# Optimization experiments

Hardware: AMD Instinct MI355X
Metric: run time of the kernel (lower is better)

The kernel has to match this reference:

```python
import math
import jax, jax.numpy as jnp
import numpy as np

N, C, H, W = 32, 128, 56, 56


def unfold3(x, axis, dil):
    """F.unfold with 3-tap kernel along `axis`, dilation `dil`, padding `dil`.
    Input (n,c,h,w) -> output (n,c,3,h,w); tap k takes offset (k-1)*dil."""
    pad_cfg = [(0, 0)] * 4
    pad_cfg[axis] = (dil, dil)
    xp = jnp.pad(x, pad_cfg)
    size = x.shape[axis]
    taps = [jax.lax.slice_in_dim(xp, k * dil, k * dil + size, axis=axis) for k in range(3)]
    return jnp.stack(taps, axis=2)


def setup_inputs() -> dict:
    key = jax.random.key(0)
    k0, k1, k2, k3, k4 = jax.random.split(key, 5)
    x = jax.random.normal(k0, (N, C, H, W), dtype=jnp.float32)
    # trunc_normal_(std=0.02) approximated by normal * 0.02
    p2 = jax.random.normal(k1, (1, 1, 3, 1, W), dtype=jnp.float32) * 0.02
    # 1x1 conv weight (out=C, in=3C), kaiming-ish scale
    p3 = jax.random.normal(k2, (C, 3 * C), dtype=jnp.float32) * (1.0 / math.sqrt(3 * C))
    p5 = jax.random.normal(k3, (1, 1, H, W), dtype=jnp.float32) * 0.02
    p10 = jax.random.normal(k4, (1, C, 3, H, W), dtype=jnp.float32) * 0.02
    return {"x": x, "p2": p2, "p3": p3, "p5": p5, "p10": p10}


def reference(x, p2, p3, p5, p10):
    n, c, h, w = x.shape
    # t_1: vertical 3-tap unfold, dilation 2 -> (n,c,3,h,w)
    t1 = unfold3(x, axis=2, dil=2)
    t2 = p2 * t1                                              # (n,c,3,h,w)
    # t_3: 1x1 conv over the c*3 channel view
    t3 = jnp.einsum('nkhw,ck->nchw', t1.reshape(n, c * 3, h, w), p3)
    # t_4: horizontal 3-tap unfold, dilation 1
    t4 = unfold3(t3, axis=3, dil=1)                           # (n,c,3,h,w)
    t5 = p5 * t3                                              # (n,c,h,w)
    # t_7/t_8: horizontal 3-tap unfold of x, dilation 2, softmax over taps
    t7 = unfold3(x, axis=3, dil=2)
    t8 = jax.nn.softmax(t7, axis=2)                           # (n,c,3,h,w)
    # t_9: bmm over spatial dim -> (n,c,c*3)
    t9 = jnp.einsum('ncx,ndx->ncd', x.reshape(n, c, h * w),
                    t4.reshape(n, c * 3, h * w)) / math.sqrt(h * w)
    t10 = p10 * t8                                            # (n,c,3,h,w)
    # t_11: memory-reinterpreting view: (n,1,c,h,w) - (n,3,c,h,w) -> back to (n,c,3,h,w)
    t11 = (t5[:, None] - t2.reshape(n, 3, c, h, w)).reshape(n, c, 3, h, w)
    t12 = t11 - t10                                           # (n,c,3,h,w)
    # t_13: bmm over c*3 -> (n,c,h*w)
    t13 = jnp.einsum('ncd,ndx->ncx', t9,
                     t12.reshape(n, c * 3, h * w)) / math.sqrt(c * 3)
    return t13.reshape(n, c, h, w)
```

## Files before the change

### kernel.cpp

```cpp
#include <hip/hip_runtime.h>
#include <stdint.h>

#define NB 32
#define C_ 128
#define H_ 56
#define W_ 56
#define HW 3136
#define KD 384

typedef __attribute__((ext_vector_type(8))) short bf16x8;
typedef __attribute__((ext_vector_type(4))) float f32x4;

__device__ inline uint16_t f2bf(float f) {
    uint32_t u = __float_as_uint(f);
    return (uint16_t)((u + 0x7FFFu + ((u >> 16) & 1u)) >> 16);
}
__device__ inline float bf2f(uint16_t b) {
    return __uint_as_float(((uint32_t)b) << 16);
}

__global__ __launch_bounds__(256) void p1_xtp(const float* __restrict__ x,
                                              uint16_t* __restrict__ xtp,
                                              uint16_t* __restrict__ xb) {
    __shared__ uint16_t lt[56][136];
    const int h = blockIdx.x, n = blockIdx.y, tid = threadIdx.x;
    const int c = tid >> 1, wh = tid & 1;
    const float* xr = &x[(((size_t)n * C_ + c) * H_ + h) * W_ + wh * 28];
    uint32_t pk[14];
#pragma unroll
    for (int q = 0; q < 7; ++q) {
        float4 v = *(const float4*)&xr[q * 4];
        int wb = wh * 28 + q * 4;
        uint16_t b0 = f2bf(v.x), b1 = f2bf(v.y), b2 = f2bf(v.z), b3 = f2bf(v.w);
        lt[wb + 0][c] = b0;
        lt[wb + 1][c] = b1;
        lt[wb + 2][c] = b2;
        lt[wb + 3][c] = b3;
        pk[q * 2]     = (uint32_t)b0 | ((uint32_t)b1 << 16);
        pk[q * 2 + 1] = (uint32_t)b2 | ((uint32_t)b3 << 16);
    }
    {
        uint16_t* xrow = &xb[(((size_t)n * C_ + c) * H_ + h) * 64 + wh * 28];
#pragma unroll
        for (int q = 0; q < 7; ++q)
            *(uint2*)&xrow[q * 4] = make_uint2(pk[q * 2], pk[q * 2 + 1]);
        if (wh == 1) {
            uint4 z = {0, 0, 0, 0};
            *(uint4*)&xrow[28] = z;
        }
    }
    __syncthreads();
    const int w = tid >> 2, qc = tid & 3;
    uint16_t* dst = &xtp[((((size_t)n * H_ + h) * 64 + w)) * C_ + qc * 32];
    if (w < 56) {
        const uint32_t* s = (const uint32_t*)&lt[w][qc * 32];
        uint4 a = *(const uint4*)(s);
        uint4 b = *(const uint4*)(s + 4);
        uint4 c4 = *(const uint4*)(s + 8);
        uint4 d4 = *(const uint4*)(s + 12);
        *(uint4*)dst = a;
        *(uint4*)(dst + 8) = b;
        *(uint4*)(dst + 16) = c4;
        *(uint4*)(dst + 24) = d4;
    } else {
        uint4 z = {0, 0, 0, 0};
        *(uint4*)dst = z;
        *(uint4*)(dst + 8) = z;
        *(uint4*)(dst + 16) = z;
        *(uint4*)(dst + 24) = z;
    }
}

__global__ __launch_bounds__(256) void kpt(const float* __restrict__ p10,
                                           const float* __restrict__ p3,
                                           uint16_t* __restrict__ p10t,
                                           uint16_t* __restrict__ ap) {
    const int h = blockIdx.x, tid = threadIdx.x;
    for (int idx = tid; idx < 3072; idx += 256) {
        int w = idx & 63, ch = idx >> 6;
        int dp0 = ch * 8;
        uint32_t pk[4];
#pragma unroll
        for (int j = 0; j < 8; ++j) {
            int dp = dp0 + j;
            int tap = dp >> 7, c2 = dp & 127;
            int dor = 3 * c2 + tap;
            float v = (w < W_) ? p10[(size_t)dor * HW + h * W_ + w] : 0.f;
            uint16_t bb = f2bf(v);
            if (j & 1) pk[j >> 1] |= ((uint32_t)bb) << 16;
            else       pk[j >> 1] = bb;
        }
        *(uint4*)&p10t[((size_t)h * 64 + w) * KD + dp0] = *(const uint4*)pk;
    }
    for (int i = h * 256 + tid; i < 49152; i += 56 * 256) {
        int c = i / KD, dp = i - c * KD;
        int tap = dp >> 7, c2 = dp & 127;
        ap[i] = f2bf(p3[c * KD + 3 * c2 + tap]);
    }
}

__global__ __launch_bounds__(256) void k1(const uint16_t* __restrict__ xtp,
                                          const uint16_t* __restrict__ ap,
                                          uint16_t* __restrict__ t3b) {
    __shared__ uint16_t smem[3 * 32 * 128];
    const int bx = blockIdx.x, n = blockIdx.y, tid = threadIdx.x;
    const int h = bx >> 1, wbase = (bx & 1) << 5;
    const int lane = tid & 63, wid = tid >> 6;
    const int c15 = lane & 15, kq = lane >> 4;

    for (int t = tid; t < 1536; t += 256) {
        int tap = t >> 9, r = t & 511, w = r >> 4, qp = r & 15;
        int q = qp ^ (w & 7);
        int hh = h + 2 * (tap - 1);
        uint4 v = {0, 0, 0, 0};
        if ((unsigned)hh < (unsigned)H_)
            v = *(const uint4*)&xtp[((((size_t)n * H_ + hh) * 64 + wbase + w)) * C_ + q * 8];
        *(uint4*)&smem[tap * 4096 + w * 128 + qp * 8] = v;
    }
    __syncthreads();

    f32x4 acc[2][2] = {};
    for (int ks = 0; ks < 12; ++ks) {
        int tap = ks >> 2, kk = ks & 3;
        bf16x8 a[2], b[2];
#pragma unroll
        for (int m = 0; m < 2; ++m) {
            int c = wid * 32 + m * 16 + c15;
            a[m] = *(const bf16x8*)&ap[c * KD + ks * 32 + kq * 8];
        }
#pragma unroll
        for (int nt = 0; nt < 2; ++nt) {
            int w = nt * 16 + c15;
            int q = kk * 4 + kq;
            b[nt] = *(const bf16x8*)&smem[tap * 4096 + w * 128 + (q ^ (w & 7)) * 8];
        }
#pragma unroll
        for (int m = 0; m < 2; ++m)
#pragma unroll
            for (int nt = 0; nt < 2; ++nt)
                acc[m][nt] = __builtin_amdgcn_mfma_f32_16x16x32_bf16(a[m], b[nt], acc[m][nt], 0, 0, 0);
    }
    __syncthreads();

    uint16_t* lrow = smem;
#pragma unroll
    for (int m = 0; m < 2; ++m)
#pragma unroll
        for (int nt = 0; nt < 2; ++nt)
#pragma unroll
            for (int r = 0; r < 4; ++r) {
                int c = wid * 32 + m * 16 + kq * 4 + r;
                int wl = nt * 16 + c15;
                lrow[c * 40 + wl] = f2bf(acc[m][nt][r]);
            }
    __syncthreads();

    const uint32_t* lrowd = (const uint32_t*)smem;
    for (int t = tid; t < 512; t += 256) {
        int c = t >> 2, ch = t & 3;
        int m0 = c * 20 + ch * 4;
        uint4 o = make_uint4(lrowd[m0], lrowd[m0 + 1], lrowd[m0 + 2], lrowd[m0 + 3]);
        *(uint4*)&t3b[(((size_t)n * C_ + c) * H_ + h) * 64 + wbase + ch * 8] = o;
    }
}

__global__ __launch_bounds__(512) void k2(const uint16_t* __restrict__ xb,
                                          const uint16_t* __restrict__ t3b,
                                          uint16_t* __restrict__ part16) {
    __shared__ uint16_t xs[32 * 64];
    __shared__ uint16_t ts[128 * 64];
    const int bx = blockIdx.x;
    const int hc = bx >> 2, cq = bx & 3;
    const int n = blockIdx.y;
    const int tid = threadIdx.x, lane = tid & 63, wid = tid >> 6;
    const int c15 = lane & 15, kq = lane >> 4;

    f32x4 acc[2][3] = {};
    for (int hr = 0; hr < 8; ++hr) {
        const int h = hc * 8 + hr;
        __syncthreads();
        if (tid < 256) {
            int cl = tid >> 3, qp = tid & 7, q = qp ^ (cl & 7);
            uint4 v = *(const uint4*)&xb[(((size_t)n * C_ + cq * 32 + cl) * H_ + h) * 64 + q * 8];
            *(uint4*)&xs[cl * 64 + qp * 8] = v;
        }
        for (int t = tid; t < 1024; t += 512) {
            int c2 = t >> 3, qp = t & 7, q = qp ^ (c2 & 7);
            uint4 v = *(const uint4*)&t3b[(((size_t)n * C_ + c2) * H_ + h) * 64 + q * 8];
            *(uint4*)&ts[c2 * 64 + qp * 8] = v;
        }
        __syncthreads();
#pragma unroll
        for (int ks = 0; ks < 2; ++ks) {
            const int q = ks * 4 + kq;
            bf16x8 a[2];
#pragma unroll
            for (int m = 0; m < 2; ++m) {
                int cl = m * 16 + c15;
                a[m] = *(const bf16x8*)&xs[cl * 64 + ((q ^ (cl & 7)) << 3)];
            }
            const int c2 = wid * 16 + c15;
            const int base = c2 * 64;
            const int s7 = c2 & 7;
            uint4 v = *(const uint4*)&ts[base + ((q ^ s7) << 3)];
            uint32_t pv = (q > 0) ? *(const uint32_t*)&ts[base + (((q - 1) ^ s7) << 3) + 6] : 0u;
            uint32_t nx = (q < 7) ? *(const uint32_t*)&ts[base + (((q + 1) ^ s7) << 3)] : 0u;
            uint4 b0, b2;
            b0.x = (v.x << 16) | (pv >> 16);
            b0.y = (v.y << 16) | (v.x >> 16);
            b0.z = (v.z << 16) | (v.y >> 16);
            b0.w = (v.w << 16) | (v.z >> 16);
            b2.x = (v.y << 16) | (v.x >> 16);
            b2.y = (v.z << 16) | (v.y >> 16);
            b2.z = (v.w << 16) | (v.z >> 16);
            b2.w = (nx << 16)  | (v.w >> 16);
            bf16x8 bt0 = *(const bf16x8*)&b0;
            bf16x8 bt1 = *(const bf16x8*)&v;
            bf16x8 bt2 = *(const bf16x8*)&b2;
#pragma unroll
            for (int m = 0; m < 2; ++m) {
                acc[m][0] = __builtin_amdgcn_mfma_f32_16x16x32_bf16(a[m], bt0, acc[m][0], 0, 0, 0);
                acc[m][1] = __builtin_amdgcn_mfma_f32_16x16x32_bf16(a[m], bt1, acc[m][1], 0, 0, 0);
                acc[m][2] = __builtin_amdgcn_mfma_f32_16x16x32_bf16(a[m], bt2, acc[m][2], 0, 0, 0);
            }
        }
    }
#pragma unroll
    for (int m = 0; m < 2; ++m)
#pragma unroll
        for (int tap = 0; tap < 3; ++tap)
#pragma unroll
            for (int r = 0; r < 4; ++r) {
                int c = cq * 32 + m * 16 + kq * 4 + r;
                int dp = tap * 128 + wid * 16 + c15;
                part16[((size_t)(hc * NB + n) * C_ + c) * 384 + dp] = f2bf(acc[m][tap][r]);
            }
}

__global__ __launch_bounds__(256) void kra(const uint16_t* __restrict__ part16,
                                           uint16_t* __restrict__ acat) {
    __shared__ uint16_t lds[4][384];
    const int tid = threadIdx.x;
    const int rl = tid >> 6, lane = tid & 63;
    const int nc = blockIdx.x * 4 + rl;
    const float sc = 1.f / 56.f;
#pragma unroll
    for (int j = 0; j < 6; ++j) {
        int dp = j * 64 + lane;
        float s = 0.f;
#pragma unroll
        for (int hc = 0; hc < 7; ++hc)
            s += bf2f(part16[((size_t)hc * NB * C_ + nc) * 384 + dp]);
        uint16_t v = f2bf(s * sc);
        acat[(size_t)nc * 512 + dp] = v;
        lds[rl][dp] = v;
    }
    __syncthreads();
#pragma unroll
    for (int t2 = 0; t2 < 2; ++t2) {
        int t = tid + t2 * 256;
        int r = t >> 7, m = t & 127;
        float s = 0.f;
#pragma unroll
        for (int r3 = 0; r3 < 3; ++r3) {
            int d = m + 128 * r3;
            int q3 = d / 3;
            int dp = (d - q3 * 3) * 128 + q3;
            s += bf2f(lds[r][dp]);
        }
        acat[(size_t)(blockIdx.x * 4 + r) * 512 + 384 + m] = f2bf(s);
    }
}

__global__ __launch_bounds__(256, 4) void k3(const uint16_t* __restrict__ xtp,
                                             const uint16_t* __restrict__ t3b,
                                             const uint16_t* __restrict__ acat,
                                             const uint16_t* __restrict__ p10t,
                                             const float* __restrict__ p2,
                                             const float* __restrict__ p5,
                                             float* __restrict__ out) {
    __shared__ uint16_t tsm[32 * 512];
    const int bx = blockIdx.x, n = blockIdx.y, tid = threadIdx.x;
    const int h = bx >> 1, wbase = (bx & 1) << 5;
    const int lane = tid & 63, wid = tid >> 6;

    {
        const int w = tid & 31, seg = tid >> 5;
        const int wg = wbase + w;
        const int wsw = w & 7;
        float p2v[3];
#pragma unroll
        for (int tap = 0; tap < 3; ++tap)
            p2v[tap] = (wg < W_) ? p2[tap * W_ + wg] : 0.f;
        const size_t xrow = ((size_t)n * H_ + h) * 64;
        const int wgm2 = (wg >= 2) ? wg - 2 : 0;
        const int wgp2 = (wg + 2 < 64) ? wg + 2 : 63;

#pragma unroll
        for (int s = 0; s < 2; ++s) {
            const int c2b = (seg + s * 8) * 8;
            bf16x8 xh_v = *(const bf16x8*)&xtp[(xrow + wg) * C_ + c2b];
            bf16x8 xm_v = *(const bf16x8*)&xtp[(xrow + wgm2) * C_ + c2b];
            bf16x8 xp_v = *(const bf16x8*)&xtp[(xrow + wgp2) * C_ + c2b];
            float sm[3][8];
#pragma unroll
            for (int j = 0; j < 8; ++j) {
                float a1 = bf2f((uint16_t)xh_v[j]);
                float a0 = (wg >= 2) ? bf2f((uint16_t)xm_v[j]) : 0.f;
                float a2 = bf2f((uint16_t)xp_v[j]);
                float mx = fmaxf(a0, fmaxf(a1, a2));
                float e0 = __expf(a0 - mx), e1 = __expf(a1 - mx), e2 = __expf(a2 - mx);
                float rs = 1.f / (e0 + e1 + e2);
                sm[0][j] = e0 * rs; sm[1][j] = e1 * rs; sm[2][j] = e2 * rs;
            }
#pragma unroll
            for (int tap = 0; tap < 3; ++tap) {
                bf16x8 xhh;
                float p2e;
                if (tap == 1) { xhh = xh_v; p2e = p2v[1]; }
                else {
                    const int hh = h + 2 * (tap - 1);
                    const bool hok = (unsigned)hh < (unsigned)H_;
                    const int hhc = hok ? hh : h;
                    xhh = *(const bf16x8*)&xtp[(((size_t)n * H_ + hhc) * 64 + wg) * C_ + c2b];
                    p2e = hok ? p2v[tap] : 0.f;
                }
                bf16x8 pv = *(const bf16x8*)&p10t[((size_t)h * 64 + wg) * KD + tap * 128 + c2b];
                uint32_t pk[4];
#pragma unroll
                for (int j = 0; j < 8; ++j) {
                    float val = -(p2e * bf2f((uint16_t)xhh[j]) + bf2f((uint16_t)pv[j]) * sm[tap][j]);
                    uint16_t bb = f2bf(val);
                    if (j & 1) pk[j >> 1] |= ((uint32_t)bb) << 16;
                    else       pk[j >> 1] = bb;
                }
                int q = (tap * 128 + c2b) >> 3;
                *(uint4*)&tsm[w * 512 + ((q ^ wsw) << 3)] = *(const uint4*)pk;
            }
        }
    }

    {
        const int c2f = tid >> 1;
        const int whl = (tid & 1) << 4;
        const uint16_t* t3r = &t3b[(((size_t)n * C_ + c2f) * H_ + h) * 64 + wbase + whl];
        const int qf = 48 + (c2f >> 3);
        const int cf7 = c2f & 7;
#pragma unroll
        for (int g = 0; g < 2; ++g) {
            bf16x8 tv = *(const bf16x8*)&t3r[g * 8];
#pragma unroll
            for (int j = 0; j < 8; ++j) {
                int wl = whl + g * 8 + j;
                int wwg = wbase + wl;
                float p5v = (wwg < W_) ? p5[h * W_ + wwg] : 0.f;
                tsm[wl * 512 + ((qf ^ (wl & 7)) << 3) + cf7] = f2bf(p5v * bf2f((uint16_t)tv[j]));
            }
        }
    }
    __syncthreads();

    const int wm = wid;
    f32x4 acc[2][2] = {};
    for (int ks = 0; ks < 16; ++ks) {
        bf16x8 a[2], b[2];
#pragma unroll
        for (int m = 0; m < 2; ++m) {
            int c = wm * 32 + m * 16 + (lane & 15);
            a[m] = *(const bf16x8*)&acat[((size_t)n * C_ + c) * 512 + ks * 32 + (lane >> 4) * 8];
        }
#pragma unroll
        for (int nt = 0; nt < 2; ++nt) {
            int wl = nt * 16 + (lane & 15);
            int q = ks * 4 + (lane >> 4);
            b[nt] = *(const bf16x8*)&tsm[wl * 512 + ((q ^ (wl & 7)) << 3)];
        }
#pragma unroll
        for (int m = 0; m < 2; ++m)
#pragma unroll
            for (int nt = 0; nt < 2; ++nt)
                acc[m][nt] = __builtin_amdgcn_mfma_f32_16x16x32_bf16(a[m], b[nt], acc[m][nt], 0, 0, 0);
    }

    const float s = 0.05103103630798287f;
#pragma unroll
    for (int m = 0; m < 2; ++m)
#pragma unroll
        for (int nt = 0; nt < 2; ++nt) {
            int wwg = wbase + nt * 16 + (lane & 15);
            if (wwg < W_) {
                int c = wm * 32 + m * 16 + (lane >> 4) * 4;
                float* dst = &out[(((size_t)n * C_ + c) * H_ + h) * W_ + wwg];
#pragma unroll
                for (int r = 0; r < 4; ++r) dst[(size_t)r * HW] = acc[m][nt][r] * s;
            }
        }
}

extern "C" void kernel_launch(void* const* d_in, const int* in_sizes, int n_in,
                              void* d_out, int out_size, void* d_ws, size_t ws_size,
                              hipStream_t stream) {
    const float* x   = (const float*)d_in[0];
    const float* p2  = (const float*)d_in[1];
    const float* p3  = (const float*)d_in[2];
    const float* p5  = (const float*)d_in[3];
    const float* p10 = (const float*)d_in[4];
    float* out = (float*)d_out;

    uint8_t* w8 = (uint8_t*)d_ws;
    uint16_t* t3b    = (uint16_t*)(w8);
    uint16_t* ap     = (uint16_t*)(w8 + 29360128);
    uint16_t* xtp    = (uint16_t*)(w8 + 29458432);
    uint16_t* xb     = (uint16_t*)(w8 + 58818560);
    uint16_t* part16 = (uint16_t*)(w8 + 88178688);
    uint16_t* acat   = (uint16_t*)(w8 + 110198784);
    uint16_t* p10t   = (uint16_t*)(w8 + 114393088);

    p1_xtp<<<dim3(H_, NB), 256, 0, stream>>>(x, xtp, xb);
    kpt<<<dim3(H_), 256, 0, stream>>>(p10, p3, p10t, ap);
    k1<<<dim3(112, NB), 256, 0, stream>>>(xtp, ap, t3b);
    k2<<<dim3(28, NB), 512, 0, stream>>>(xb, t3b, part16);
    kra<<<dim3(1024), 256, 0, stream>>>(part16, acat);
    k3<<<dim3(112, NB), 256, 0, stream>>>(xtp, t3b, acat, p10t, p2, p5, out);
}
```

Before: 219.9 us.

## Batch global loads ahead of LDS stores and process two rows per sync

In k1 all six global loads for the staging tile are issued into registers before any LDS store, so more memory requests are in flight at once. In k2 two h-rows are staged per barrier pair into doubled shared buffers, which halves the number of __syncthreads and lets more loads overlap. In the final kernel every x and p10 vector for both segments is loaded up front before the softmax and combine math, which improves memory-level parallelism. The cost is higher register pressure and double the LDS in k2, which may reduce occupancy.

Measured after the change: 212.8 us. 3.2% less time.

```diff
diff --git a/kernel.cpp b/kernel.cpp
--- a/kernel.cpp
+++ b/kernel.cpp
@@ -108,14 +108,23 @@
     const int lane = tid & 63, wid = tid >> 6;
     const int c15 = lane & 15, kq = lane >> 4;
 
-    for (int t = tid; t < 1536; t += 256) {
+    uint4 vst[6];
+#pragma unroll
+    for (int i = 0; i < 6; ++i) {
+        int t = i * 256 + tid;
         int tap = t >> 9, r = t & 511, w = r >> 4, qp = r & 15;
         int q = qp ^ (w & 7);
         int hh = h + 2 * (tap - 1);
         uint4 v = {0, 0, 0, 0};
         if ((unsigned)hh < (unsigned)H_)
             v = *(const uint4*)&xtp[((((size_t)n * H_ + hh) * 64 + wbase + w)) * C_ + q * 8];
-        *(uint4*)&smem[tap * 4096 + w * 128 + qp * 8] = v;
+        vst[i] = v;
+    }
+#pragma unroll
+    for (int i = 0; i < 6; ++i) {
+        int t = i * 256 + tid;
+        int tap = t >> 9, r = t & 511, w = r >> 4, qp = r & 15;
+        *(uint4*)&smem[tap * 4096 + w * 128 + qp * 8] = vst[i];
     }
     __syncthreads();
 
@@ -167,8 +176,8 @@
 __global__ __launch_bounds__(512) void k2(const uint16_t* __restrict__ xb,
                                           const uint16_t* __restrict__ t3b,
                                           uint16_t* __restrict__ part16) {
-    __shared__ uint16_t xs[32 * 64];
-    __shared__ uint16_t ts[128 * 64];
+    __shared__ uint16_t xs[2][32 * 64];
+    __shared__ uint16_t ts[2][128 * 64];
     const int bx = blockIdx.x;
     const int hc = bx >> 2, cq = bx & 3;
     const int n = blockIdx.y;
@@ -176,52 +185,60 @@
     const int c15 = lane & 15, kq = lane >> 4;
 
     f32x4 acc[2][3] = {};
-    for (int hr = 0; hr < 8; ++hr) {
-        const int h = hc * 8 + hr;
+    for (int hr = 0; hr < 8; hr += 2) {
         __syncthreads();
-        if (tid < 256) {
-            int cl = tid >> 3, qp = tid & 7, q = qp ^ (cl & 7);
-            uint4 v = *(const uint4*)&xb[(((size_t)n * C_ + cq * 32 + cl) * H_ + h) * 64 + q * 8];
-            *(uint4*)&xs[cl * 64 + qp * 8] = v;
-        }
-        for (int t = tid; t < 1024; t += 512) {
-            int c2 = t >> 3, qp = t & 7, q = qp ^ (c2 & 7);
-            uint4 v = *(const uint4*)&t3b[(((size_t)n * C_ + c2) * H_ + h) * 64 + q * 8];
-            *(uint4*)&ts[c2 * 64 + qp * 8] = v;
+#pragma unroll
+        for (int hp = 0; hp < 2; ++hp) {
+            const int h = hc * 8 + hr + hp;
+            if (tid < 256) {
+                int cl = tid >> 3, qp = tid & 7, q = qp ^ (cl & 7);
+                uint4 v = *(const uint4*)&xb[(((size_t)n * C_ + cq * 32 + cl) * H_ + h) * 64 + q * 8];
+                *(uint4*)&xs[hp][cl * 64 + qp * 8] = v;
+            }
+#pragma unroll
+            for (int i = 0; i < 2; ++i) {
+                int t = i * 512 + tid;
+                int c2 = t >> 3, qp = t & 7, q = qp ^ (c2 & 7);
+                uint4 v = *(const uint4*)&t3b[(((size_t)n * C_ + c2) * H_ + h) * 64 + q * 8];
+                *(uint4*)&ts[hp][c2 * 64 + qp * 8] = v;
+            }
         }
         __syncthreads();
 #pragma unroll
-        for (int ks = 0; ks < 2; ++ks) {
-            const int q = ks * 4 + kq;
-            bf16x8 a[2];
-#pragma unroll
-            for (int m = 0; m < 2; ++m) {
-                int cl = m * 16 + c15;
-                a[m] = *(const bf16x8*)&xs[cl * 64 + ((q ^ (cl & 7)) << 3)];
-            }
-            const int c2 = wid * 16 + c15;
-            const int base = c2 * 64;
-            const int s7 = c2 & 7;
-            uint4 v = *(const uint4*)&ts[base + ((q ^ s7) << 3)];
-            uint32_t pv = (q > 0) ? *(const uint32_t*)&ts[base + (((q - 1) ^ s7) << 3) + 6] : 0u;
-            uint32_t nx = (q < 7) ? *(const uint32_t*)&ts[base + (((q + 1) ^ s7) << 3)] : 0u;
-            uint4 b0, b2;
-            b0.x = (v.x << 16) | (pv >> 16);
-            b0.y = (v.y << 16) | (v.x >> 16);
-            b0.z = (v.z << 16) | (v.y >> 16);
-            b0.w = (v.w << 16) | (v.z >> 16);
-            b2.x = (v.y << 16) | (v.x >> 16);
-            b2.y = (v.z << 16) | (v.y >> 16);
-            b2.z = (v.w << 16) | (v.z >> 16);
-            b2.w = (nx << 16)  | (v.w >> 16);
-            bf16x8 bt0 = *(const bf16x8*)&b0;
-            bf16x8 bt1 = *(const bf16x8*)&v;
-            bf16x8 bt2 = *(const bf16x8*)&b2;
-#pragma unroll
-            for (int m = 0; m < 2; ++m) {
-                acc[m][0] = __builtin_amdgcn_mfma_f32_16x16x32_bf16(a[m], bt0, acc[m][0], 0, 0, 0);
-                acc[m][1] = __builtin_amdgcn_mfma_f32_16x16x32_bf16(a[m], bt1, acc[m][1], 0, 0, 0);
-                acc[m][2] = __builtin_amdgcn_mfma_f32_16x16x32_bf16(a[m], bt2, acc[m][2], 0, 0, 0);
+        for (int hp = 0; hp < 2; ++hp) {
+#pragma unroll
+            for (int ks = 0; ks < 2; ++ks) {
+                const int q = ks * 4 + kq;
+                bf16x8 a[2];
+#pragma unroll
+                for (int m = 0; m < 2; ++m) {
+                    int cl = m * 16 + c15;
+                    a[m] = *(const bf16x8*)&xs[hp][cl * 64 + ((q ^ (cl & 7)) << 3)];
+                }
+                const int c2 = wid * 16 + c15;
+                const int base = c2 * 64;
+                const int s7 = c2 & 7;
+                uint4 v = *(const uint4*)&ts[hp][base + ((q ^ s7) << 3)];
+                uint32_t pv = (q > 0) ? *(const uint32_t*)&ts[hp][base + (((q - 1) ^ s7) << 3) + 6] : 0u;
+                uint32_t nx = (q < 7) ? *(const uint32_t*)&ts[hp][base + (((q + 1) ^ s7) << 3)] : 0u;
+                uint4 b0, b2;
+                b0.x = (v.x << 16) | (pv >> 16);
+                b0.y = (v.y << 16) | (v.x >> 16);
+                b0.z = (v.z << 16) | (v.y >> 16);
+                b0.w = (v.w << 16) | (v.z >> 16);
+                b2.x = (v.y << 16) | (v.x >> 16);
+                b2.y = (v.z << 16) | (v.y >> 16);
+                b2.z = (v.w << 16) | (v.z >> 16);
+                b2.w = (nx << 16)  | (v.w >> 16);
+                bf16x8 bt0 = *(const bf16x8*)&b0;
+                bf16x8 bt1 = *(const bf16x8*)&v;
+                bf16x8 bt2 = *(const bf16x8*)&b2;
+#pragma unroll
+                for (int m = 0; m < 2; ++m) {
+                    acc[m][0] = __builtin_amdgcn_mfma_f32_16x16x32_bf16(a[m], bt0, acc[m][0], 0, 0, 0);
+                    acc[m][1] = __builtin_amdgcn_mfma_f32_16x16x32_bf16(a[m], bt1, acc[m][1], 0, 0, 0);
+                    acc[m][2] = __builtin_amdgcn_mfma_f32_16x16x32_bf16(a[m], bt2, acc[m][2], 0, 0, 0);
+                }
             }
         }
     }
@@ -295,48 +312,57 @@
         const size_t xrow = ((size_t)n * H_ + h) * 64;
         const int wgm2 = (wg >= 2) ? wg - 2 : 0;
         const int wgp2 = (wg + 2 < 64) ? wg + 2 : 63;
-
+        const int hh0 = h - 2, hh2 = h + 2;
+        const bool hok0 = (hh0 >= 0), hok2 = (hh2 < H_);
+        const size_t xrow0 = ((size_t)n * H_ + (hok0 ? hh0 : h)) * 64;
+        const size_t xrow2 = ((size_t)n * H_ + (hok2 ? hh2 : h)) * 64;
+        const float p2e0 = hok0 ? p2v[0] : 0.f;
+        const float p2e2 = hok2 ? p2v[2] : 0.f;
+        const uint16_t* pt = &p10t[((size_t)h * 64 + wg) * KD];
+
+        bf16x8 Lxh[2], Lxm[2], Lxp[2], Lx0[2], Lx2[2], Lp0[2], Lp1[2], Lp2[2];
 #pragma unroll
         for (int s = 0; s < 2; ++s) {
             const int c2b = (seg + s * 8) * 8;
-            bf16x8 xh_v = *(const bf16x8*)&xtp[(xrow + wg) * C_ + c2b];
-            bf16x8 xm_v = *(const bf16x8*)&xtp[(xrow + wgm2) * C_ + c2b];
-            bf16x8 xp_v = *(const bf16x8*)&xtp[(xrow + wgp2) * C_ + c2b];
+            Lxh[s] = *(const bf16x8*)&xtp[(xrow + wg) * C_ + c2b];
+            Lxm[s] = *(const bf16x8*)&xtp[(xrow + wgm2) * C_ + c2b];
+            Lxp[s] = *(const bf16x8*)&xtp[(xrow + wgp2) * C_ + c2b];
+            Lx0[s] = *(const bf16x8*)&xtp[(xrow0 + wg) * C_ + c2b];
+            Lx2[s] = *(const bf16x8*)&xtp[(xrow2 + wg) * C_ + c2b];
+            Lp0[s] = *(const bf16x8*)&pt[c2b];
+            Lp1[s] = *(const bf16x8*)&pt[128 + c2b];
+            Lp2[s] = *(const bf16x8*)&pt[256 + c2b];
+        }
+#pragma unroll
+        for (int s = 0; s < 2; ++s) {
+            const int c2b = (seg + s * 8) * 8;
             float sm[3][8];
 #pragma unroll
             for (int j = 0; j < 8; ++j) {
-                float a1 = bf2f((uint16_t)xh_v[j]);
-                float a0 = (wg >= 2) ? bf2f((uint16_t)xm_v[j]) : 0.f;
-                float a2 = bf2f((uint16_t)xp_v[j]);
+                float a1 = bf2f((uint16_t)Lxh[s][j]);
+                float a0 = (wg >= 2) ? bf2f((uint16_t)Lxm[s][j]) : 0.f;
+                float a2 = bf2f((uint16_t)Lxp[s][j]);
                 float mx = fmaxf(a0, fmaxf(a1, a2));
                 float e0 = __expf(a0 - mx), e1 = __expf(a1 - mx), e2 = __expf(a2 - mx);
                 float rs = 1.f / (e0 + e1 + e2);
                 sm[0][j] = e0 * rs; sm[1][j] = e1 * rs; sm[2][j] = e2 * rs;
             }
-#pragma unroll
-            for (int tap = 0; tap < 3; ++tap) {
-                bf16x8 xhh;
-                float p2e;
-                if (tap == 1) { xhh = xh_v; p2e = p2v[1]; }
-                else {
-                    const int hh = h + 2 * (tap - 1);
-                    const bool hok = (unsigned)hh < (unsigned)H_;
-                    const int hhc = hok ? hh : h;
-                    xhh = *(const bf16x8*)&xtp[(((size_t)n * H_ + hhc) * 64 + wg) * C_ + c2b];
-                    p2e = hok ? p2v[tap] : 0.f;
-                }
-                bf16x8 pv = *(const bf16x8*)&p10t[((size_t)h * 64 + wg) * KD + tap * 128 + c2b];
-                uint32_t pk[4];
-#pragma unroll
-                for (int j = 0; j < 8; ++j) {
-                    float val = -(p2e * bf2f((uint16_t)xhh[j]) + bf2f((uint16_t)pv[j]) * sm[tap][j]);
-                    uint16_t bb = f2bf(val);
-                    if (j & 1) pk[j >> 1] |= ((uint32_t)bb) << 16;
-                    else       pk[j >> 1] = bb;
-                }
-                int q = (tap * 128 + c2b) >> 3;
-                *(uint4*)&tsm[w * 512 + ((q ^ wsw) << 3)] = *(const uint4*)pk;
-            }
+            uint32_t pk0[4], pk1[4], pk2[4];
+#pragma unroll
+            for (int j = 0; j < 8; ++j) {
+                float v0 = -(p2e0   * bf2f((uint16_t)Lx0[s][j]) + bf2f((uint16_t)Lp0[s][j]) * sm[0][j]);
+                float v1 = -(p2v[1] * bf2f((uint16_t)Lxh[s][j]) + bf2f((uint16_t)Lp1[s][j]) * sm[1][j]);
+                float v2 = -(p2e2   * bf2f((uint16_t)Lx2[s][j]) + bf2f((uint16_t)Lp2[s][j]) * sm[2][j]);
+                uint16_t b0 = f2bf(v0), b1 = f2bf(v1), b2 = f2bf(v2);
+                if (j & 1) { pk0[j >> 1] |= ((uint32_t)b0) << 16;
+                             pk1[j >> 1] |= ((uint32_t)b1) << 16;
+                             pk2[j >> 1] |= ((uint32_t)b2) << 16; }
+                else       { pk0[j >> 1] = b0; pk1[j >> 1] = b1; pk2[j >> 1] = b2; }
+            }
+            int q0 = (c2b) >> 3, q1 = (128 + c2b) >> 3, q2 = (256 + c2b) >> 3;
+            *(uint4*)&tsm[w * 512 + ((q0 ^ wsw) << 3)] = *(const uint4*)pk0;
+            *(uint4*)&tsm[w * 512 + ((q1 ^ wsw) << 3)] = *(const uint4*)pk1;
+            *(uint4*)&tsm[w * 512 + ((q2 ^ wsw) << 3)] = *(const uint4*)pk2;
         }
     }
 
```
